# Kernel tuning notes

Measured on AMD Instinct MI355X. Metric: run time of the kernel, lower is better.

## Reference

```python
import jax, jax.numpy as jnp
import numpy as np


def setup_inputs() -> dict:
    key = jax.random.key(0)
    k1, k2, k3, k4, k5, k6 = jax.random.split(key, 6)
    B, V = 128, 128000
    logits = jax.random.normal(k1, (B, V), dtype=jnp.float32) * 2.0
    # keep temperatures away from 0 to avoid overflow in logits/temp
    temperatures = 0.7 + 0.6 * jax.random.uniform(k2, (B,), dtype=jnp.float32)
    top_ks = jax.random.randint(k3, (B,), 1, 1024, dtype=jnp.int32)
    top_ps = 0.7 + 0.29 * jax.random.uniform(k4, (B,), dtype=jnp.float32)
    min_ps = 0.02 * jax.random.uniform(k5, (B,), dtype=jnp.float32)
    # uniform variate for inverse-CDF multinomial sampling (one sample per row)
    u = jax.random.uniform(k6, (B, 1), dtype=jnp.float32)
    return {
        "logits": logits,
        "temperatures": temperatures,
        "top_ks": top_ks,
        "top_ps": top_ps,
        "min_ps": min_ps,
        "u": u,
    }


def reference(logits, temperatures, top_ks, top_ps, min_ps, u):
    """Faithful jax version of Sampler's torch-native sampling path:
    softmax(logits/T) -> descending sort -> top-k mask -> top-p mask
    (cumsum computed pre-mask, exactly as torch code) -> min-p mask ->
    multinomial sample (inverse CDF with provided uniform u) ->
    gather original token index. Also returns the renormalized filtered
    probs scattered back to vocab order (top_p_normalize_probs-style)."""
    B, V = logits.shape
    probs = jax.nn.softmax(logits / temperatures[:, None], axis=-1)  # [B, V]

    order = jnp.argsort(-probs, axis=-1)                     # descending indices
    probs_sort = jnp.take_along_axis(probs, order, axis=-1)  # [B, V] sorted desc
    probs_sum = jnp.cumsum(probs_sort, axis=-1)              # cumsum BEFORE masking

    pos = jnp.arange(V, dtype=jnp.int32)[None, :]
    # top-k: zero everything at rank >= top_k
    probs_sort = jnp.where(pos >= top_ks[:, None], 0.0, probs_sort)
    # top-p: zero where cumulative mass strictly before this token exceeds top_p
    probs_sort = jnp.where(probs_sum - probs_sort > top_ps[:, None], 0.0, probs_sort)
    # min-p: threshold relative to the max prob (rank-0 entry survives both masks)
    min_p_thr = probs_sort[:, :1] * min_ps[:, None]
    probs_sort = jnp.where(probs_sort < min_p_thr, 0.0, probs_sort)

    total = jnp.sum(probs_sort, axis=-1, keepdims=True)      # [B, 1]
    cdf = jnp.cumsum(probs_sort, axis=-1) / total            # normalized CDF
    # inverse-CDF sampling == torch.multinomial(probs_sort, 1)
    sampled_rank = jnp.clip(jnp.sum(cdf < u, axis=-1, keepdims=True), 0, V - 1)
    token_ids = jnp.take_along_axis(order, sampled_rank, axis=-1)[:, 0].astype(jnp.int32)

    # scatter renormalized filtered probs back to original vocab positions
    inv_order = jnp.argsort(order, axis=-1)
    norm_probs = jnp.take_along_axis(probs_sort / total, inv_order, axis=-1)
    return token_ids, norm_probs
```

## Files before the change

kernel.cpp:

```cpp
#include <hip/hip_runtime.h>
#include <stdint.h>
#include <math.h>

#define TPB 1024
#define NB 2048
#define SPLIT 4
#define LCAND 2560
#define CAND2 2048
#define PS 4096
#define L2E 1.44269504088896f

typedef float vfloat4 __attribute__((ext_vector_type(4)));
typedef unsigned long long ull;

__device__ __forceinline__ unsigned fkey(float f) {
    unsigned u = __float_as_uint(f);
    return (u & 0x80000000u) ? ~u : (u | 0x80000000u);
}
__device__ __forceinline__ float funkey(unsigned k) {
    unsigned u = (k & 0x80000000u) ? (k ^ 0x80000000u) : ~k;
    return __uint_as_float(u);
}
__device__ __forceinline__ ull packkv(unsigned k, unsigned idx) {
    return ((ull)k << 32) | (ull)(~idx);
}

__device__ __forceinline__ void suffix_scan_2048(unsigned* h, unsigned* wscr, int tid)
{
    const int lane = tid & 63, w = tid >> 6;
    const int i0 = 2047 - 2 * tid;
    const int i1 = 2046 - 2 * tid;
    unsigned a = h[i0], b = h[i1];
    unsigned s = a + b;
    unsigned inc = s;
    #pragma unroll
    for (int d = 1; d < 64; d <<= 1) { unsigned o = __shfl_up(inc, d); if (lane >= d) inc += o; }
    if (lane == 63) wscr[w] = inc;
    __syncthreads();
    if (w == 0) {
        unsigned v = (lane < 16) ? wscr[lane] : 0u;
        unsigned vi = v;
        #pragma unroll
        for (int d = 1; d < 16; d <<= 1) { unsigned o = __shfl_up(vi, d); if (lane >= d) vi += o; }
        if (lane < 16) wscr[16 + lane] = vi - v;
    }
    __syncthreads();
    unsigned off = wscr[16 + w] + (inc - s);
    h[i0] = off + a;
    h[i1] = off + a + b;
    __syncthreads();
}

__global__ __launch_bounds__(TPB)
void k1_scan(const float* __restrict__ logits,
             const float* __restrict__ temps,
             const int* __restrict__ top_ks,
             float* __restrict__ out_probs,
             float* __restrict__ ws_ms,
             unsigned* __restrict__ ws_cut,
             unsigned* __restrict__ ws_cnt,
             ull* __restrict__ ws_cand,
             int V, int Vq)
{
    const int blk = blockIdx.x;
    const int b = blk / SPLIT, s = blk % SPLIT;
    const int tid = threadIdx.x, lane = tid & 63, w = tid >> 6;
    const int start = s * Vq;
    const int len = min(Vq, V - start);
    const int slot = blk;
    const float invT = 1.0f / temps[b];
    int K = top_ks[b]; K = max(K, 1); K = min(K, 1024);

    __shared__ unsigned hist[NB];
    __shared__ unsigned uscr[32];
    __shared__ float fred[32];
    __shared__ unsigned cnt;
    __shared__ int bstar;

    if (len <= 0) {
        if (tid == 0) {
            ws_ms[4*slot] = -1e30f; ws_ms[4*slot+1] = 0.0f; ws_ms[4*slot+2] = -1e30f;
            ws_cut[slot] = 0u; ws_cnt[slot] = 0u;
        }
        return;
    }

    for (int i = tid; i < NB; i += TPB) hist[i] = 0;
    if (tid == 0) { cnt = 0; bstar = 0; }
    __syncthreads();

    const float* __restrict__ row = logits + (size_t)b * V + start;
    const vfloat4* __restrict__ row4 = (const vfloat4*)row;
    float* __restrict__ orow = out_probs + (size_t)b * V + start;
    vfloat4* __restrict__ orow4 = (vfloat4*)orow;
    const int L4 = len >> 2;

    const int nps = min(len, PS);
    float m0 = -1e30f;
    for (int i = tid; i < nps; i += TPB) {
        float lv = row[i];
        m0 = fmaxf(m0, lv);
        atomicAdd(&hist[fkey(lv) >> 21], 1u);
    }
    #pragma unroll
    for (int d = 32; d > 0; d >>= 1) m0 = fmaxf(m0, __shfl_down(m0, d));
    if (lane == 0) fred[w] = m0;
    __syncthreads();
    if (tid == 0) {
        float mm = fred[0];
        for (int j = 1; j < 16; ++j) mm = fmaxf(mm, fred[j]);
        fred[16] = mm;
    }
    __syncthreads();
    const float m0max = fred[16];

    suffix_scan_2048(hist, uscr, tid);
    unsigned TGT = (unsigned)((K * 13) / 64 + 16);
    if (TGT > (unsigned)nps) TGT = (unsigned)nps;
    for (int e = tid; e < NB; e += TPB) {
        unsigned Se = hist[e];
        unsigned Sn = (e < NB - 1) ? hist[e + 1] : 0u;
        if (Se >= TGT && Sn < TGT) bstar = e;
    }
    __syncthreads();
    const unsigned cutkey = (unsigned)bstar << 21;
    const float cutval = funkey(cutkey);

    const float ca = invT * L2E;
    const float cb = -m0max * invT * L2E;

    float z = 0.0f, mb = -1e30f;
    ull* gc = ws_cand + (size_t)slot * LCAND;
    const vfloat4 z4 = (vfloat4)0.0f;

    for (int i = tid; i < L4; i += TPB) {
        vfloat4 v = row4[i];
        __builtin_nontemporal_store(z4, &orow4[i]);
        float x0 = v[0], x1 = v[1], x2 = v[2], x3 = v[3];
        z += exp2f(fmaf(x0, ca, cb)) + exp2f(fmaf(x1, ca, cb))
           + exp2f(fmaf(x2, ca, cb)) + exp2f(fmaf(x3, ca, cb));
        mb = fmaxf(mb, fmaxf(fmaxf(x0, x1), fmaxf(x2, x3)));
        bool c0 = x0 >= cutval, c1 = x1 >= cutval, c2 = x2 >= cutval, c3 = x3 >= cutval;
        if (c0 | c1 | c2 | c3) {
            int n = (int)c0 + (int)c1 + (int)c2 + (int)c3;
            unsigned base = atomicAdd(&cnt, (unsigned)n);
            unsigned bi = (unsigned)(start + (i << 2));
            if (c0) { if (base < LCAND) gc[base] = packkv(fkey(x0), bi + 0); base++; }
            if (c1) { if (base < LCAND) gc[base] = packkv(fkey(x1), bi + 1); base++; }
            if (c2) { if (base < LCAND) gc[base] = packkv(fkey(x2), bi + 2); base++; }
            if (c3) { if (base < LCAND) gc[base] = packkv(fkey(x3), bi + 3); base++; }
        }
    }
    for (int i = (L4 << 2) + tid; i < len; i += TPB) {
        float lv = row[i];
        __builtin_nontemporal_store(0.0f, &orow[i]);
        z += exp2f(fmaf(lv, ca, cb));
        mb = fmaxf(mb, lv);
        if (lv >= cutval) {
            unsigned base = atomicAdd(&cnt, 1u);
            if (base < LCAND) gc[base] = packkv(fkey(lv), (unsigned)(start + i));
        }
    }
    __syncthreads();
    #pragma unroll
    for (int d = 32; d > 0; d >>= 1) {
        z += __shfl_down(z, d);
        mb = fmaxf(mb, __shfl_down(mb, d));
    }
    if (lane == 0) { fred[w] = z; fred[16 + w] = mb; }
    __syncthreads();
    if (tid == 0) {
        float zz = 0.0f, mm = -1e30f;
        for (int j = 0; j < 16; ++j) { zz += fred[j]; mm = fmaxf(mm, fred[16 + j]); }
        ws_ms[4*slot + 0] = m0max * invT;
        ws_ms[4*slot + 1] = zz;
        ws_ms[4*slot + 2] = mm * invT;
        ws_cut[slot] = cutkey;
        ws_cnt[slot] = cnt;
    }
}

__global__ __launch_bounds__(TPB)
void k2_sample(const float* __restrict__ logits,
               const float* __restrict__ temps,
               const int* __restrict__ top_ks,
               const float* __restrict__ top_ps,
               const float* __restrict__ min_ps,
               const float* __restrict__ uvec,
               const float* __restrict__ ws_ms,
               const unsigned* __restrict__ ws_cut,
               const unsigned* __restrict__ ws_cnt,
               const ull* __restrict__ ws_cand,
               float* __restrict__ out_tok,
               float* __restrict__ out_probs,
               int V)
{
    const int b = blockIdx.x;
    const int tid = threadIdx.x, lane = tid & 63, w = tid >> 6;
    const float invT = 1.0f / temps[b];
    int Korig = top_ks[b]; Korig = max(Korig, 1); Korig = min(Korig, 1024);
    const unsigned Ku = (unsigned)Korig;
    const float top_p = top_ps[b], min_p = min_ps[b], uval = uvec[b];

    __shared__ __align__(16) char smem[53504];
    ull*            cand  = (ull*)(smem);
    ull*            cand2 = (ull*)(smem + 16384);
    unsigned*       hist  = (unsigned*)(smem + 32768);
    unsigned short* cnts  = (unsigned short*)(smem + 41216);
    float*          sh_p  = (float*)(smem + 45312);
    float*          sh_c  = (float*)(smem + 49408);
    __shared__ unsigned uscr[32];
    __shared__ float fws[32];
    __shared__ unsigned scnt;
    __shared__ int sh_i1, sh_i2;
    __shared__ unsigned sh_u1;

    float Cy[SPLIT], zq[SPLIT], Mbyq[SPLIT];
    unsigned cutq[SPLIT], cntq[SPLIT];
    #pragma unroll
    for (int q = 0; q < SPLIT; ++q) {
        int sl = b * SPLIT + q;
        Cy[q] = ws_ms[4*sl]; zq[q] = ws_ms[4*sl+1]; Mbyq[q] = ws_ms[4*sl+2];
        cutq[q] = ws_cut[sl]; cntq[q] = ws_cnt[sl];
    }
    float Y = -1e30f;
    #pragma unroll
    for (int q = 0; q < SPLIT; ++q) Y = fmaxf(Y, Cy[q]);
    float Z = 0.0f;
    #pragma unroll
    for (int q = 0; q < SPLIT; ++q)
        if (zq[q] > 0.0f) Z += zq[q] * exp2f((Cy[q] - Y) * L2E);

    bool fb = false;
    #pragma unroll
    for (int q = 0; q < SPLIT; ++q) {
        if (cntq[q] > (unsigned)LCAND) fb = true;
        if (Mbyq[q] - Cy[q] > 60.0f) fb = true;
    }
    unsigned cutmax = 0;
    #pragma unroll
    for (int q = 0; q < SPLIT; ++q) cutmax = max(cutmax, cutq[q]);

    unsigned Tkey = 0;
    int count = 0;

    if (!fb) {
        for (int i = tid; i < NB; i += TPB) hist[i] = 0;
        if (tid == 0) { sh_i1 = -1; sh_i2 = -1; }
        __syncthreads();
        #pragma unroll
        for (int q = 0; q < SPLIT; ++q) {
            const ull* gc = ws_cand + (size_t)(b * SPLIT + q) * LCAND;
            int nl = min((int)cntq[q], LCAND);
            for (int i = tid; i < nl; i += TPB)
                atomicAdd(&hist[(unsigned)(gc[i] >> 32) >> 21], 1u);
        }
        __syncthreads();
        suffix_scan_2048(hist, uscr, tid);
        for (int e = tid; e < NB; e += TPB) {
            unsigned Se = hist[e], Sn = (e < NB-1) ? hist[e+1] : 0u;
            if (Se >= Ku && Sn < Ku) { sh_i1 = e; sh_u1 = Sn; }
        }
        __syncthreads();
        int b1 = sh_i1;
        unsigned cab = sh_u1;
        if (b1 < 0) fb = true;
        else {
            for (int i = tid; i < NB; i += TPB) hist[i] = 0;
            __syncthreads();
            #pragma unroll
            for (int q = 0; q < SPLIT; ++q) {
                const ull* gc = ws_cand + (size_t)(b * SPLIT + q) * LCAND;
                int nl = min((int)cntq[q], LCAND);
                for (int i = tid; i < nl; i += TPB) {
                    unsigned k = (unsigned)(gc[i] >> 32);
                    if ((int)(k >> 21) == b1) atomicAdd(&hist[(k >> 10) & (NB - 1)], 1u);
                }
            }
            __syncthreads();
            suffix_scan_2048(hist, uscr, tid);
            for (int e = tid; e < NB; e += TPB) {
                unsigned Se = cab + hist[e];
                unsigned Sn = cab + ((e < NB-1) ? hist[e+1] : 0u);
                if (Se >= Ku && Sn < Ku) sh_i2 = e;
            }
            __syncthreads();
            if (sh_i2 < 0) fb = true;
            else {
                Tkey = ((unsigned)b1 << 21) | ((unsigned)sh_i2 << 10);
                if (Tkey < cutmax) fb = true;
            }
        }
    }
    if (!fb) {
        if (tid == 0) scnt = 0;
        __syncthreads();
        #pragma unroll
        for (int q = 0; q < SPLIT; ++q) {
            const ull* gc = ws_cand + (size_t)(b * SPLIT + q) * LCAND;
            int nl = min((int)cntq[q], LCAND);
            for (int i = tid; i < nl; i += TPB) {
                ull e = gc[i];
                if ((unsigned)(e >> 32) >= Tkey) {
                    unsigned pos = atomicAdd(&scnt, 1u);
                    if (pos < CAND2) cand[pos] = e;
                }
            }
        }
        __syncthreads();
        if (scnt > (unsigned)CAND2 || scnt < Ku) fb = true;
        else count = (int)scnt;
    }

    if (fb) {
        const float* __restrict__ row = logits + (size_t)b * V;
        float m = -1e30f, z = 0.0f;
        for (int i = tid; i < V; i += TPB) {
            float y = row[i] * invT;
            float nm = fmaxf(m, y);
            z = z * exp2f((m - nm) * L2E) + exp2f((y - nm) * L2E);
            m = nm;
        }
        sh_p[tid] = m; sh_c[tid] = z;
        __syncthreads();
        for (int d = TPB >> 1; d > 0; d >>= 1) {
            if (tid < d) {
                float m1 = sh_p[tid], z1 = sh_c[tid];
                float m2 = sh_p[tid + d], z2 = sh_c[tid + d];
                float mm = fmaxf(m1, m2);
                sh_c[tid] = z1 * exp2f((m1 - mm) * L2E) + z2 * exp2f((m2 - mm) * L2E);
                sh_p[tid] = mm;
            }
            __syncthreads();
        }
        Y = sh_p[0]; Z = sh_c[0];
        __syncthreads();
        for (int i = tid; i < NB; i += TPB) hist[i] = 0;
        __syncthreads();
        for (int i = tid; i < V; i += TPB) atomicAdd(&hist[fkey(row[i]) >> 21], 1u);
        __syncthreads();
        suffix_scan_2048(hist, uscr, tid);
        for (int e = tid; e < NB; e += TPB) {
            unsigned Se = hist[e], Sn = (e < NB-1) ? hist[e+1] : 0u;
            if (Se >= Ku && Sn < Ku) { sh_i1 = e; sh_u1 = Sn; }
        }
        __syncthreads();
        int b1 = sh_i1;
        unsigned cab = sh_u1;
        for (int i = tid; i < NB; i += TPB) hist[i] = 0;
        __syncthreads();
        for (int i = tid; i < V; i += TPB) {
            unsigned k = fkey(row[i]);
            if ((int)(k >> 21) == b1) atomicAdd(&hist[(k >> 10) & (NB - 1)], 1u);
        }
        __syncthreads();
        suffix_scan_2048(hist, uscr, tid);
        for (int e = tid; e < NB; e += TPB) {
            unsigned Se = cab + hist[e];
            unsigned Sn = cab + ((e < NB-1) ? hist[e+1] : 0u);
            if (Se >= Ku && Sn < Ku) sh_i2 = e;
        }
        __syncthreads();
        Tkey = ((unsigned)b1 << 21) | ((unsigned)sh_i2 << 10);
        if (tid == 0) scnt = 0;
        __syncthreads();
        for (int i = tid; i < V; i += TPB) {
            unsigned k = fkey(row[i]);
            if (k >= Tkey) {
                unsigned pos = atomicAdd(&scnt, 1u);
                if (pos < CAND2) cand[pos] = packkv(k, (unsigned)i);
            }
        }
        __syncthreads();
        count = (scnt < (unsigned)CAND2) ? (int)scnt : CAND2;
    }

    int K = min(Korig, count);

    unsigned mk = 0;
    for (int i = tid; i < count; i += TPB) mk = max(mk, (unsigned)(cand[i] >> 32));
    #pragma unroll
    for (int d = 32; d > 0; d >>= 1) mk = max(mk, __shfl_down(mk, d));
    if (lane == 0) uscr[w] = mk;
    __syncthreads();
    if (tid == 0) {
        unsigned m2 = 0;
        for (int j = 0; j < 16; ++j) m2 = max(m2, uscr[j]);
        uscr[16] = m2;
    }
    __syncthreads();
    const unsigned maxkey = uscr[16];
    const unsigned range = maxkey - Tkey;
    int shift = 0;
    while ((range >> shift) > (NB - 1)) shift++;

    for (int i = tid; i <= NB; i += TPB) hist[i] = 0;
    __syncthreads();
    for (int i = tid; i < count; i += TPB)
        atomicAdd(&hist[((unsigned)(cand[i] >> 32) - Tkey) >> shift], 1u);
    __syncthreads();
    unsigned mc = 0;
    for (int i = tid; i < NB; i += TPB) {
        unsigned h = hist[i];
        cnts[i] = (unsigned short)h;
        mc = max(mc, h);
    }
    #pragma unroll
    for (int d = 32; d > 0; d >>= 1) mc = max(mc, __shfl_down(mc, d));
    if (lane == 0) uscr[w] = mc;
    __syncthreads();
    if (tid == 0) {
        unsigned m2 = 0;
        for (int j = 0; j < 16; ++j) m2 = max(m2, uscr[j]);
        uscr[17] = m2;
    }
    __syncthreads();
    const bool use_bitonic = (uscr[17] > 48u);
    ull* srt;
    if (!use_bitonic) {
        suffix_scan_2048(hist, uscr, tid);
        for (int i = tid; i < count; i += TPB) {
            ull v = cand[i];
            unsigned bin = ((unsigned)(v >> 32) - Tkey) >> shift;
            unsigned pos = atomicAdd(&hist[bin + 1], 1u);
            cand2[pos] = v;
        }
        __syncthreads();
        for (int bn = tid; bn < NB; bn += TPB) {
            int c = (int)cnts[bn];
            if (c >= 2) {
                int st = (int)hist[bn + 1] - c;
                for (int x = 1; x < c; ++x) {
                    ull key = cand2[st + x];
                    int y = x - 1;
                    while (y >= 0 && cand2[st + y] < key) { cand2[st + y + 1] = cand2[st + y]; --y; }
                    cand2[st + y + 1] = key;
                }
            }
        }
        __syncthreads();
        srt = cand2;
    } else {
        int n_sort = 1;
        while (n_sort < count) n_sort <<= 1;
        for (int i = tid; i < n_sort; i += TPB)
            if (i >= count) cand[i] = 0ull;
        __syncthreads();
        for (int kk = 2; kk <= n_sort; kk <<= 1) {
            for (int j = kk >> 1; j > 0; j >>= 1) {
                for (int i = tid; i < n_sort; i += TPB) {
                    int ixj = i ^ j;
                    if (ixj > i) {
                        ull a = cand[i], c = cand[ixj];
                        bool up = (i & kk) == 0;
                        if (up ? (a < c) : (a > c)) { cand[i] = c; cand[ixj] = a; }
                    }
                }
                __syncthreads();
            }
        }
        srt = cand;
    }

    float pv = 0.0f;
    if (tid < K) {
        unsigned k = (unsigned)(srt[tid] >> 32);
        pv = exp2f((funkey(k) * invT - Y) * L2E) / Z;
    }
    float inc = pv;
    #pragma unroll
    for (int d = 1; d < 64; d <<= 1) { float o = __shfl_up(inc, d); if (lane >= d) inc += o; }
    if (lane == 63) fws[w] = inc;
    __syncthreads();
    if (w == 0) {
        float v = (lane < 16) ? fws[lane] : 0.0f;
        float vi = v;
        #pragma unroll
        for (int d = 1; d < 16; d <<= 1) { float o = __shfl_up(vi, d); if (lane >= d) vi += o; }
        if (lane < 16) fws[16 + lane] = vi - v;
    }
    __syncthreads();
    float cum = inc + fws[16 + w];
    sh_p[tid] = pv;
    sh_c[tid] = cum;
    if (tid == 0) sh_i1 = K;
    __syncthreads();

    if (tid < K) {
        float excl = cum - pv;
        if (excl > top_p) atomicMin(&sh_i1, tid);
    }
    __syncthreads();
    int n1 = sh_i1;
    float thr = sh_p[0] * min_p;
    if (tid == 0) sh_i2 = n1;
    __syncthreads();
    if (tid < n1 && sh_p[tid] < thr) atomicMin(&sh_i2, tid);
    __syncthreads();
    int nf = sh_i2;
    float total = sh_c[nf - 1];

    int pred = (tid < nf) && ((sh_c[tid] / total) < uval);
    int rank = __syncthreads_count(pred);
    if (rank > nf - 1) rank = nf - 1;
    if (rank < 0) rank = 0;
    if (tid == 0)
        out_tok[b] = (float)(~(unsigned)(srt[rank] & 0xFFFFFFFFull));

    if (tid < nf) {
        unsigned idx = ~(unsigned)(srt[tid] & 0xFFFFFFFFull);
        out_probs[(size_t)b * V + idx] = sh_p[tid] / total;
    }
}

extern "C" void kernel_launch(void* const* d_in, const int* in_sizes, int n_in,
                              void* d_out, int out_size, void* d_ws, size_t ws_size,
                              hipStream_t stream) {
    const float* logits = (const float*)d_in[0];
    const float* temps  = (const float*)d_in[1];
    const int*   top_ks = (const int*)d_in[2];
    const float* top_ps = (const float*)d_in[3];
    const float* min_ps = (const float*)d_in[4];
    const float* u      = (const float*)d_in[5];
    const int B = in_sizes[1];
    const int V = in_sizes[0] / B;
    float* out_tok   = (float*)d_out;
    float* out_probs = out_tok + B;

    int Vq = (((V + SPLIT - 1) / SPLIT) + 3) & ~3;

    char* ws = (char*)d_ws;
    size_t off = 0;
    auto take = [&](size_t bytes) { char* p = ws + off; off = (off + bytes + 255) & ~(size_t)255; return p; };
    float*    ws_ms   = (float*)take((size_t)B * SPLIT * 4 * sizeof(float));
    unsigned* ws_cut  = (unsigned*)take((size_t)B * SPLIT * sizeof(unsigned));
    unsigned* ws_cnt  = (unsigned*)take((size_t)B * SPLIT * sizeof(unsigned));
    ull*      ws_cand = (ull*)take((size_t)B * SPLIT * LCAND * sizeof(ull));
    (void)ws_size;

    k1_scan<<<dim3(SPLIT * B), dim3(TPB), 0, stream>>>(
        logits, temps, top_ks, out_probs, ws_ms, ws_cut, ws_cnt, ws_cand, V, Vq);
    k2_sample<<<dim3(B), dim3(TPB), 0, stream>>>(
        logits, temps, top_ks, top_ps, min_ps, u, ws_ms, ws_cut, ws_cnt, ws_cand,
        out_tok, out_probs, V);
}
```

Measured before the change: 166.1 us.

## Split output zeroing into dedicated blocks and streamline candidate selection sort

The first kernel now launches three times as many blocks: two of every three only zero the output probability buffer with regular stores, and the rest do the logit scan without writing zeros. The candidate cut target is now derived from the expected per-slice count with a variance margin rather than a fixed fraction of K. In the sampling kernel, the two-level radix threshold search plus separate bucket sort is replaced by a single histogram over the key range taken from per-slice max keys. That histogram picks the threshold and places candidates straight into buckets for insertion sort, with bitonic sort kept only for the fallback path. This aims to cut passes over shared memory and separate the store-bound zeroing from the compute-bound scan, at the cost of more blocks and a tighter candidate margin that could trigger the slow fallback more often.

```diff
diff --git a/kernel.cpp b/kernel.cpp
--- a/kernel.cpp
+++ b/kernel.cpp
@@ -56,18 +56,33 @@
              const float* __restrict__ temps,
              const int* __restrict__ top_ks,
              float* __restrict__ out_probs,
-             float* __restrict__ ws_ms,
+             float* __restrict__ ws_meta,
              unsigned* __restrict__ ws_cut,
              unsigned* __restrict__ ws_cnt,
              ull* __restrict__ ws_cand,
-             int V, int Vq)
+             int V, int Vq, int n)
 {
     const int blk = blockIdx.x;
-    const int b = blk / SPLIT, s = blk % SPLIT;
     const int tid = threadIdx.x, lane = tid & 63, w = tid >> 6;
+    const int role = blk % 3;
+
+    if (role != 0) {
+        const int ZB = (gridDim.x / 3) * 2;
+        const int zid = (blk / 3) * 2 + (role - 1);
+        const int n4 = n >> 2;
+        vfloat4* p4 = (vfloat4*)out_probs;
+        const vfloat4 z4 = (vfloat4)0.0f;
+        const int step = ZB * TPB;
+        for (int i = zid * TPB + tid; i < n4; i += step) p4[i] = z4;
+        for (int i = (n4 << 2) + zid * TPB + tid; i < n; i += step) out_probs[i] = 0.0f;
+        return;
+    }
+
+    const int sblk = blk / 3;
+    const int b = sblk / SPLIT, s = sblk % SPLIT;
     const int start = s * Vq;
     const int len = min(Vq, V - start);
-    const int slot = blk;
+    const int slot = sblk;
     const float invT = 1.0f / temps[b];
     int K = top_ks[b]; K = max(K, 1); K = min(K, 1024);
 
@@ -79,7 +94,8 @@
 
     if (len <= 0) {
         if (tid == 0) {
-            ws_ms[4*slot] = -1e30f; ws_ms[4*slot+1] = 0.0f; ws_ms[4*slot+2] = -1e30f;
+            ws_meta[4*slot] = -1e30f; ws_meta[4*slot+1] = 0.0f;
+            ws_meta[4*slot+2] = -1e30f; ws_meta[4*slot+3] = __uint_as_float(0u);
             ws_cut[slot] = 0u; ws_cnt[slot] = 0u;
         }
         return;
@@ -91,8 +107,6 @@
 
     const float* __restrict__ row = logits + (size_t)b * V + start;
     const vfloat4* __restrict__ row4 = (const vfloat4*)row;
-    float* __restrict__ orow = out_probs + (size_t)b * V + start;
-    vfloat4* __restrict__ orow4 = (vfloat4*)orow;
     const int L4 = len >> 2;
 
     const int nps = min(len, PS);
@@ -115,7 +129,8 @@
     const float m0max = fred[16];
 
     suffix_scan_2048(hist, uscr, tid);
-    unsigned TGT = (unsigned)((K * 13) / 64 + 16);
+    float sexp = (float)K * (float)nps / (float)V;
+    unsigned TGT = (unsigned)(sexp + 6.0f * sqrtf(sexp) + 16.5f);
     if (TGT > (unsigned)nps) TGT = (unsigned)nps;
     for (int e = tid; e < NB; e += TPB) {
         unsigned Se = hist[e];
@@ -131,19 +146,17 @@
 
     float z = 0.0f, mb = -1e30f;
     ull* gc = ws_cand + (size_t)slot * LCAND;
-    const vfloat4 z4 = (vfloat4)0.0f;
 
     for (int i = tid; i < L4; i += TPB) {
         vfloat4 v = row4[i];
-        __builtin_nontemporal_store(z4, &orow4[i]);
         float x0 = v[0], x1 = v[1], x2 = v[2], x3 = v[3];
         z += exp2f(fmaf(x0, ca, cb)) + exp2f(fmaf(x1, ca, cb))
            + exp2f(fmaf(x2, ca, cb)) + exp2f(fmaf(x3, ca, cb));
         mb = fmaxf(mb, fmaxf(fmaxf(x0, x1), fmaxf(x2, x3)));
         bool c0 = x0 >= cutval, c1 = x1 >= cutval, c2 = x2 >= cutval, c3 = x3 >= cutval;
         if (c0 | c1 | c2 | c3) {
-            int n = (int)c0 + (int)c1 + (int)c2 + (int)c3;
-            unsigned base = atomicAdd(&cnt, (unsigned)n);
+            int nh = (int)c0 + (int)c1 + (int)c2 + (int)c3;
+            unsigned base = atomicAdd(&cnt, (unsigned)nh);
             unsigned bi = (unsigned)(start + (i << 2));
             if (c0) { if (base < LCAND) gc[base] = packkv(fkey(x0), bi + 0); base++; }
             if (c1) { if (base < LCAND) gc[base] = packkv(fkey(x1), bi + 1); base++; }
@@ -153,7 +166,6 @@
     }
     for (int i = (L4 << 2) + tid; i < len; i += TPB) {
         float lv = row[i];
-        __builtin_nontemporal_store(0.0f, &orow[i]);
         z += exp2f(fmaf(lv, ca, cb));
         mb = fmaxf(mb, lv);
         if (lv >= cutval) {
@@ -172,9 +184,10 @@
     if (tid == 0) {
         float zz = 0.0f, mm = -1e30f;
         for (int j = 0; j < 16; ++j) { zz += fred[j]; mm = fmaxf(mm, fred[16 + j]); }
-        ws_ms[4*slot + 0] = m0max * invT;
-        ws_ms[4*slot + 1] = zz;
-        ws_ms[4*slot + 2] = mm * invT;
+        ws_meta[4*slot + 0] = m0max * invT;
+        ws_meta[4*slot + 1] = zz;
+        ws_meta[4*slot + 2] = mm * invT;
+        ws_meta[4*slot + 3] = __uint_as_float(fkey(mm));
         ws_cut[slot] = cutkey;
         ws_cnt[slot] = cnt;
     }
@@ -187,7 +200,7 @@
                const float* __restrict__ top_ps,
                const float* __restrict__ min_ps,
                const float* __restrict__ uvec,
-               const float* __restrict__ ws_ms,
+               const float* __restrict__ ws_meta,
                const unsigned* __restrict__ ws_cut,
                const unsigned* __restrict__ ws_cnt,
                const ull* __restrict__ ws_cand,
@@ -216,11 +229,12 @@
     __shared__ unsigned sh_u1;
 
     float Cy[SPLIT], zq[SPLIT], Mbyq[SPLIT];
-    unsigned cutq[SPLIT], cntq[SPLIT];
+    unsigned cutq[SPLIT], cntq[SPLIT], mkq[SPLIT];
     #pragma unroll
     for (int q = 0; q < SPLIT; ++q) {
         int sl = b * SPLIT + q;
-        Cy[q] = ws_ms[4*sl]; zq[q] = ws_ms[4*sl+1]; Mbyq[q] = ws_ms[4*sl+2];
+        Cy[q] = ws_meta[4*sl]; zq[q] = ws_meta[4*sl+1]; Mbyq[q] = ws_meta[4*sl+2];
+        mkq[q] = __float_as_uint(ws_meta[4*sl+3]);
         cutq[q] = ws_cut[sl]; cntq[q] = ws_cnt[sl];
     }
     float Y = -1e30f;
@@ -232,84 +246,101 @@
         if (zq[q] > 0.0f) Z += zq[q] * exp2f((Cy[q] - Y) * L2E);
 
     bool fb = false;
+    unsigned cutmax = 0, mincut = 0xFFFFFFFFu, maxkey = 0;
     #pragma unroll
     for (int q = 0; q < SPLIT; ++q) {
         if (cntq[q] > (unsigned)LCAND) fb = true;
-        if (Mbyq[q] - Cy[q] > 60.0f) fb = true;
-    }
-    unsigned cutmax = 0;
-    #pragma unroll
-    for (int q = 0; q < SPLIT; ++q) cutmax = max(cutmax, cutq[q]);
-
-    unsigned Tkey = 0;
-    int count = 0;
+        if (cntq[q] > 0u) {
+            if (Mbyq[q] - Cy[q] > 60.0f) fb = true;
+            cutmax = max(cutmax, cutq[q]);
+            mincut = min(mincut, cutq[q]);
+            maxkey = max(maxkey, mkq[q]);
+        }
+    }
+    if (mincut == 0xFFFFFFFFu) fb = true;
+
+    const unsigned base = mincut;
+    const unsigned range = maxkey - base;
+    int shift = 0;
+    while ((range >> shift) > (unsigned)(NB - 1)) shift++;
+
+    unsigned Tkeyb = 0;
+    int count = 0, bstar = 0;
 
     if (!fb) {
-        for (int i = tid; i < NB; i += TPB) hist[i] = 0;
-        if (tid == 0) { sh_i1 = -1; sh_i2 = -1; }
+        for (int i = tid; i <= NB; i += TPB) hist[i] = 0;
+        if (tid == 0) { sh_i1 = -1; scnt = 0; }
         __syncthreads();
         #pragma unroll
         for (int q = 0; q < SPLIT; ++q) {
             const ull* gc = ws_cand + (size_t)(b * SPLIT + q) * LCAND;
             int nl = min((int)cntq[q], LCAND);
             for (int i = tid; i < nl; i += TPB)
-                atomicAdd(&hist[(unsigned)(gc[i] >> 32) >> 21], 1u);
-        }
-        __syncthreads();
+                atomicAdd(&hist[((unsigned)(gc[i] >> 32) - base) >> shift], 1u);
+        }
+        __syncthreads();
+        unsigned fat = 0;
+        for (int i = tid; i < NB; i += TPB) {
+            unsigned h = hist[i];
+            cnts[i] = (unsigned short)h;
+            fat = max(fat, h);
+        }
+        #pragma unroll
+        for (int d = 32; d > 0; d >>= 1) fat = max(fat, __shfl_down(fat, d));
+        if (lane == 0) uscr[w] = fat;
+        __syncthreads();
+        if (tid == 0) {
+            unsigned m2 = 0;
+            for (int j = 0; j < 16; ++j) m2 = max(m2, uscr[j]);
+            uscr[16] = m2;
+        }
+        __syncthreads();
+        if (uscr[16] > 64u) fb = true;
+    }
+    if (!fb) {
         suffix_scan_2048(hist, uscr, tid);
         for (int e = tid; e < NB; e += TPB) {
-            unsigned Se = hist[e], Sn = (e < NB-1) ? hist[e+1] : 0u;
-            if (Se >= Ku && Sn < Ku) { sh_i1 = e; sh_u1 = Sn; }
-        }
-        __syncthreads();
-        int b1 = sh_i1;
-        unsigned cab = sh_u1;
-        if (b1 < 0) fb = true;
+            unsigned Se = hist[e], Sn = (e < NB - 1) ? hist[e + 1] : 0u;
+            if (Se >= Ku && Sn < Ku) { sh_i1 = e; sh_u1 = Se; }
+        }
+        __syncthreads();
+        if (sh_i1 < 0) fb = true;
         else {
-            for (int i = tid; i < NB; i += TPB) hist[i] = 0;
-            __syncthreads();
-            #pragma unroll
-            for (int q = 0; q < SPLIT; ++q) {
-                const ull* gc = ws_cand + (size_t)(b * SPLIT + q) * LCAND;
-                int nl = min((int)cntq[q], LCAND);
-                for (int i = tid; i < nl; i += TPB) {
-                    unsigned k = (unsigned)(gc[i] >> 32);
-                    if ((int)(k >> 21) == b1) atomicAdd(&hist[(k >> 10) & (NB - 1)], 1u);
-                }
-            }
-            __syncthreads();
-            suffix_scan_2048(hist, uscr, tid);
-            for (int e = tid; e < NB; e += TPB) {
-                unsigned Se = cab + hist[e];
-                unsigned Sn = cab + ((e < NB-1) ? hist[e+1] : 0u);
-                if (Se >= Ku && Sn < Ku) sh_i2 = e;
-            }
-            __syncthreads();
-            if (sh_i2 < 0) fb = true;
-            else {
-                Tkey = ((unsigned)b1 << 21) | ((unsigned)sh_i2 << 10);
-                if (Tkey < cutmax) fb = true;
-            }
+            bstar = sh_i1;
+            count = (int)sh_u1;
+            Tkeyb = base + ((unsigned)bstar << shift);
+            if (Tkeyb < cutmax || count > CAND2) fb = true;
         }
     }
     if (!fb) {
-        if (tid == 0) scnt = 0;
-        __syncthreads();
         #pragma unroll
         for (int q = 0; q < SPLIT; ++q) {
             const ull* gc = ws_cand + (size_t)(b * SPLIT + q) * LCAND;
             int nl = min((int)cntq[q], LCAND);
             for (int i = tid; i < nl; i += TPB) {
                 ull e = gc[i];
-                if ((unsigned)(e >> 32) >= Tkey) {
-                    unsigned pos = atomicAdd(&scnt, 1u);
-                    if (pos < CAND2) cand[pos] = e;
+                unsigned k = (unsigned)(e >> 32);
+                if (k >= Tkeyb) {
+                    unsigned bin = (k - base) >> shift;
+                    unsigned pos = atomicAdd(&hist[bin + 1], 1u);
+                    cand2[pos] = e;
                 }
             }
         }
         __syncthreads();
-        if (scnt > (unsigned)CAND2 || scnt < Ku) fb = true;
-        else count = (int)scnt;
+        for (int e = bstar + tid; e < NB; e += TPB) {
+            int c = (int)cnts[e];
+            if (c >= 2) {
+                int st = (int)hist[e + 1] - c;
+                for (int x = 1; x < c; ++x) {
+                    ull key = cand2[st + x];
+                    int y = x - 1;
+                    while (y >= 0 && cand2[st + y] < key) { cand2[st + y + 1] = cand2[st + y]; --y; }
+                    cand2[st + y + 1] = key;
+                }
+            }
+        }
+        __syncthreads();
     }
 
     if (fb) {
@@ -336,6 +367,7 @@
         Y = sh_p[0]; Z = sh_c[0];
         __syncthreads();
         for (int i = tid; i < NB; i += TPB) hist[i] = 0;
+        if (tid == 0) { sh_i1 = 0; sh_i2 = 0; sh_u1 = 0; }
         __syncthreads();
         for (int i = tid; i < V; i += TPB) atomicAdd(&hist[fkey(row[i]) >> 21], 1u);
         __syncthreads();
@@ -361,7 +393,7 @@
             if (Se >= Ku && Sn < Ku) sh_i2 = e;
         }
         __syncthreads();
-        Tkey = ((unsigned)b1 << 21) | ((unsigned)sh_i2 << 10);
+        unsigned Tkey = ((unsigned)b1 << 21) | ((unsigned)sh_i2 << 10);
         if (tid == 0) scnt = 0;
         __syncthreads();
         for (int i = tid; i < V; i += TPB) {
@@ -373,74 +405,7 @@
         }
         __syncthreads();
         count = (scnt < (unsigned)CAND2) ? (int)scnt : CAND2;
-    }
-
-    int K = min(Korig, count);
-
-    unsigned mk = 0;
-    for (int i = tid; i < count; i += TPB) mk = max(mk, (unsigned)(cand[i] >> 32));
-    #pragma unroll
-    for (int d = 32; d > 0; d >>= 1) mk = max(mk, __shfl_down(mk, d));
-    if (lane == 0) uscr[w] = mk;
-    __syncthreads();
-    if (tid == 0) {
-        unsigned m2 = 0;
-        for (int j = 0; j < 16; ++j) m2 = max(m2, uscr[j]);
-        uscr[16] = m2;
-    }
-    __syncthreads();
-    const unsigned maxkey = uscr[16];
-    const unsigned range = maxkey - Tkey;
-    int shift = 0;
-    while ((range >> shift) > (NB - 1)) shift++;
-
-    for (int i = tid; i <= NB; i += TPB) hist[i] = 0;
-    __syncthreads();
-    for (int i = tid; i < count; i += TPB)
-        atomicAdd(&hist[((unsigned)(cand[i] >> 32) - Tkey) >> shift], 1u);
-    __syncthreads();
-    unsigned mc = 0;
-    for (int i = tid; i < NB; i += TPB) {
-        unsigned h = hist[i];
-        cnts[i] = (unsigned short)h;
-        mc = max(mc, h);
-    }
-    #pragma unroll
-    for (int d = 32; d > 0; d >>= 1) mc = max(mc, __shfl_down(mc, d));
-    if (lane == 0) uscr[w] = mc;
-    __syncthreads();
-    if (tid == 0) {
-        unsigned m2 = 0;
-        for (int j = 0; j < 16; ++j) m2 = max(m2, uscr[j]);
-        uscr[17] = m2;
-    }
-    __syncthreads();
-    const bool use_bitonic = (uscr[17] > 48u);
-    ull* srt;
-    if (!use_bitonic) {
-        suffix_scan_2048(hist, uscr, tid);
-        for (int i = tid; i < count; i += TPB) {
-            ull v = cand[i];
-            unsigned bin = ((unsigned)(v >> 32) - Tkey) >> shift;
-            unsigned pos = atomicAdd(&hist[bin + 1], 1u);
-            cand2[pos] = v;
-        }
-        __syncthreads();
-        for (int bn = tid; bn < NB; bn += TPB) {
-            int c = (int)cnts[bn];
-            if (c >= 2) {
-                int st = (int)hist[bn + 1] - c;
-                for (int x = 1; x < c; ++x) {
-                    ull key = cand2[st + x];
-                    int y = x - 1;
-                    while (y >= 0 && cand2[st + y] < key) { cand2[st + y + 1] = cand2[st + y]; --y; }
-                    cand2[st + y + 1] = key;
-                }
-            }
-        }
-        __syncthreads();
-        srt = cand2;
-    } else {
+
         int n_sort = 1;
         while (n_sort < count) n_sort <<= 1;
         for (int i = tid; i < n_sort; i += TPB)
@@ -459,8 +424,10 @@
                 __syncthreads();
             }
         }
-        srt = cand;
-    }
+    }
+
+    ull* srt = fb ? cand : cand2;
+    int K = min(Korig, count);
 
     float pv = 0.0f;
     if (tid < K) {
@@ -528,19 +495,20 @@
     float* out_probs = out_tok + B;
 
     int Vq = (((V + SPLIT - 1) / SPLIT) + 3) & ~3;
+    int n = B * V;
 
     char* ws = (char*)d_ws;
     size_t off = 0;
     auto take = [&](size_t bytes) { char* p = ws + off; off = (off + bytes + 255) & ~(size_t)255; return p; };
-    float*    ws_ms   = (float*)take((size_t)B * SPLIT * 4 * sizeof(float));
+    float*    ws_meta = (float*)take((size_t)B * SPLIT * 4 * sizeof(float));
     unsigned* ws_cut  = (unsigned*)take((size_t)B * SPLIT * sizeof(unsigned));
     unsigned* ws_cnt  = (unsigned*)take((size_t)B * SPLIT * sizeof(unsigned));
     ull*      ws_cand = (ull*)take((size_t)B * SPLIT * LCAND * sizeof(ull));
     (void)ws_size;
 
-    k1_scan<<<dim3(SPLIT * B), dim3(TPB), 0, stream>>>(
-        logits, temps, top_ks, out_probs, ws_ms, ws_cut, ws_cnt, ws_cand, V, Vq);
+    k1_scan<<<dim3(3 * SPLIT * B), dim3(TPB), 0, stream>>>(
+        logits, temps, top_ks, out_probs, ws_meta, ws_cut, ws_cnt, ws_cand, V, Vq, n);
     k2_sample<<<dim3(B), dim3(TPB), 0, stream>>>(
-        logits, temps, top_ks, top_ps, min_ps, u, ws_ms, ws_cut, ws_cnt, ws_cand,
+        logits, temps, top_ks, top_ps, min_ps, u, ws_meta, ws_cut, ws_cnt, ws_cand,
         out_tok, out_probs, V);
 }
```

Result: faster. 155.5 us (-6.4%).
